# Kernel tuning notes

Hardware: AMD Instinct MI355X
Metric: run time of the kernel (lower is better)

Reference implementation:

```python
import jax, jax.numpy as jnp
import numpy as np

NV = 1_000_000   # number of 'var' nodes
NC = 500_000     # number of 'con' nodes
E = 16_000_000   # number of v2c edges (c2v is the reverse edge set)
H = 10           # n_h_feats


def setup_inputs() -> dict:
    key = jax.random.key(0)
    ks = jax.random.split(key, 24)
    s = 0.1  # weight init scale
    inp = {
        "var_c": jax.random.normal(ks[0], (NV,), jnp.float32),
        "var_x": jax.random.normal(ks[1], (NV,), jnp.float32),
        "con_b": jax.random.normal(ks[2], (NC,), jnp.float32),
        "A": jax.random.uniform(ks[3], (E,), jnp.float32),
        "src": jax.random.randint(ks[4], (E,), 0, NV, jnp.int32),
        "dst": jax.random.randint(ks[5], (E,), 0, NC, jnp.int32),
        # var_emb / con_emb Linear params
        "Wv": jax.random.normal(ks[6], (2, H), jnp.float32) * s,
        "bv": jnp.zeros((H,), jnp.float32),
        "Wc": jax.random.normal(ks[7], (1, H), jnp.float32) * s,
        "bc": jnp.zeros((H,), jnp.float32),
        # conv1 (GraphConv, shared across v2c/c2v) -- note: its output is
        # overwritten in the original forward and never reaches the output
        "W1": jax.random.normal(ks[8], (H, H), jnp.float32) * s,
        "b1": jnp.zeros((H,), jnp.float32),
        # conv2 (GraphConv, shared across v2c/c2v)
        "W2": jax.random.normal(ks[9], (H, H), jnp.float32) * s,
        "b2": jnp.zeros((H,), jnp.float32),
        # output MLP
        "Wo1": jax.random.normal(ks[10], (H, H), jnp.float32) * s,
        "bo1": jnp.zeros((H,), jnp.float32),
        "Wo2": jax.random.normal(ks[11], (H, H), jnp.float32) * s,
        "bo2": jnp.zeros((H,), jnp.float32),
        "Wo3": jax.random.normal(ks[12], (H, 1), jnp.float32) * s,
        "bo3": jnp.zeros((1,), jnp.float32),
    }
    return inp


def _gconv(x_src, W, b, s_idx, d_idx, ew, norm_src, norm_dst, n_dst):
    # DGL GraphConv, norm='both', with edge weights; in==out feats so W first.
    h = (x_src * norm_src) @ W                      # [N_src, H]
    msg = h[s_idx] * ew[:, None]                    # gather + edge weight
    agg = jax.ops.segment_sum(msg, d_idx, num_segments=n_dst)
    return agg * norm_dst + b


def reference(var_c, var_x, con_b, A, src, dst,
              Wv, bv, Wc, bc, W1, b1, W2, b2,
              Wo1, bo1, Wo2, bo2, Wo3, bo3):
    # symmetric norm from UNWEIGHTED degrees (DGL GraphConv norm='both'),
    # clamped at 1. v2c: out-deg(var), in-deg(con); c2v is the reverse.
    ones_e = jnp.ones_like(A)
    deg_v = jnp.clip(jax.ops.segment_sum(ones_e, src, num_segments=NV), 1.0)
    deg_c = jnp.clip(jax.ops.segment_sum(ones_e, dst, num_segments=NC), 1.0)
    norm_v = deg_v[:, None] ** -0.5
    norm_c = deg_c[:, None] ** -0.5

    # node embeddings
    var_feats = jnp.stack([var_c, var_x], axis=1)   # [NV, 2]
    X_var = jax.nn.relu(var_feats @ Wv + bv)        # [NV, H]
    X_con = jax.nn.relu(con_b[:, None] @ Wc + bc)   # [NC, H] (unused by convs: GraphConv ignores dst feats)

    # In the original forward, conv1 outputs (h_con / h_var) are immediately
    # overwritten by conv2 outputs (GraphConv only consumes src features),
    # so only conv2 lies on the effective compute path.
    h_con = jax.nn.relu(_gconv(X_var, W2, b2, src, dst, A, norm_v, norm_c, NC))
    h_var = jax.nn.relu(_gconv(h_con, W2, b2, dst, src, A, norm_c, norm_v, NV))

    h = jax.nn.relu(h_var @ Wo1 + bo1)
    h = jax.nn.relu(h @ Wo2 + bo2)
    logit = h @ Wo3 + bo3                           # [NV, 1]
    # dgl.readout_nodes(op='mean', ntype='var'), single graph -> [1, 1]
    return jnp.mean(logit, axis=0, keepdims=True)
```

## Files before the change

### kernel.cpp

```cpp
#include <hip/hip_runtime.h>

#define HF 10
#define ST 16
#define BST 16
#define SLC 256
#define NBINS 2048
#define VPB 512
#define TILE 12288


__global__ __launch_bounds__(1024) void k_hist(const int* __restrict__ idx,
                                               unsigned* __restrict__ hist,
                                               long long s_begin, long long s_end,
                                               int per, int shift) {
    __shared__ unsigned l[NBINS];
    int t = threadIdx.x, sl = blockIdx.x;
    for (int b = t; b < NBINS; b += 1024) l[b] = 0u;
    __syncthreads();
    long long s0 = s_begin + (long long)sl * per;
    long long s1 = s0 + per; if (s1 > s_end) s1 = s_end;
    for (long long i = s0 + t; i < s1; i += 1024)
        atomicAdd(&l[((unsigned)idx[i]) >> shift], 1u);
    __syncthreads();
    unsigned* out = hist + (size_t)sl * NBINS;
    for (int b = t; b < NBINS; b += 1024) out[b] = l[b];
}

__global__ void k_coltot(const unsigned* __restrict__ h, unsigned* __restrict__ colT) {
    int b = blockIdx.x * 256 + threadIdx.x;
    unsigned s = 0u;
    for (int sl = 0; sl < SLC; sl++) s += h[(size_t)sl * NBINS + b];
    colT[b] = s;
}

__global__ __launch_bounds__(1024) void k_prefix(const unsigned* __restrict__ colT,
                                                 unsigned* __restrict__ start) {
    __shared__ unsigned p[1024];
    int t = threadIdx.x;
    uint2 v = *(const uint2*)(colT + 2 * t);
    unsigned own = v.x + v.y;
    p[t] = own;
    __syncthreads();
    for (int off = 1; off < 1024; off <<= 1) {
        unsigned u = (t >= off) ? p[t - off] : 0u;
        __syncthreads();
        p[t] += u;
        __syncthreads();
    }
    unsigned e = p[t] - own;
    *(uint2*)(start + 2 * t) = make_uint2(e, e + v.x);
    if (t == 1023) start[NBINS] = p[1023];
}

__global__ void k_offs(unsigned* __restrict__ h, const unsigned* __restrict__ start) {
    int b = blockIdx.x * 256 + threadIdx.x;
    unsigned cur = start[b];
    for (int sl = 0; sl < SLC; sl++) {
        unsigned* cell = h + (size_t)sl * NBINS + b;
        unsigned v = *cell;
        *cell = cur;
        cur += v;
    }
}

__global__ __launch_bounds__(1024) void k_scatS2(
        const int* __restrict__ src, const int* __restrict__ dst,
        const float* __restrict__ A, const unsigned* __restrict__ offs,
        uint2* __restrict__ ebufS, long long E, int per) {
    __shared__ unsigned cur[NBINS];
    __shared__ unsigned th[NBINS];
    __shared__ unsigned tf[NBINS];
    __shared__ unsigned sc[1024];
    __shared__ __align__(16) uint2 buf[TILE];
    int t = threadIdx.x, sl = blockIdx.x;
    const unsigned* o = offs + (size_t)sl * NBINS;
    for (int b = t; b < NBINS; b += 1024) cur[b] = o[b];
    long long s0 = (long long)sl * per;
    long long s1 = s0 + per; if (s1 > E) s1 = E;
    for (long long tb = s0; tb < s1; tb += TILE) {
        int n = (int)((s1 - tb < (long long)TILE) ? (s1 - tb) : (long long)TILE);
        for (int b = t; b < NBINS; b += 1024) th[b] = 0u;
        __syncthreads();
        for (int i = t; i < n; i += 1024)
            atomicAdd(&th[((unsigned)src[tb + i]) >> 9], 1u);
        __syncthreads();
        unsigned a0 = th[2 * t], a1 = th[2 * t + 1];
        unsigned own = a0 + a1;
        sc[t] = own;
        __syncthreads();
        for (int off = 1; off < 1024; off <<= 1) {
            unsigned u = (t >= off) ? sc[t - off] : 0u;
            __syncthreads();
            sc[t] += u;
            __syncthreads();
        }
        unsigned ex = sc[t] - own;
        th[2 * t] = ex;     th[2 * t + 1] = ex + a0;
        tf[2 * t] = ex;     tf[2 * t + 1] = ex + a0;
        __syncthreads();
        for (int i = t; i < n; i += 1024) {
            unsigned s = (unsigned)src[tb + i], d = (unsigned)dst[tb + i];
            float a = A[tb + i];
            unsigned p = atomicAdd(&tf[s >> 9], 1u);
            buf[p] = make_uint2(((s & 511u) << 19) | d, __float_as_uint(a));
        }
        __syncthreads();
        int w = t >> 6, ln = t & 63;
        for (int b = w; b < NBINS; b += 16) {
            unsigned lo = th[b], cnt = tf[b] - lo, gb = cur[b];
            for (unsigned j = ln; j < cnt; j += 64)
                ebufS[gb + j] = buf[lo + j];
        }
        __syncthreads();
        for (int b = t; b < NBINS; b += 1024) cur[b] += tf[b] - th[b];
        __syncthreads();
    }
}

__global__ void k_cntS2(const uint2* __restrict__ ebufS, const unsigned* __restrict__ startS,
                        const float* __restrict__ var_c, const float* __restrict__ var_x,
                        float4* __restrict__ vcx, int NV) {
    __shared__ unsigned cnt[VPB];
    int t = threadIdx.x, b = blockIdx.x;
    cnt[t] = 0u; cnt[t + 256] = 0u;
    __syncthreads();
    unsigned i0 = startS[b], i1 = startS[b + 1];
    for (unsigned i = i0 + t; i < i1; i += 256)
        atomicAdd(&cnt[ebufS[i].x >> 19], 1u);
    __syncthreads();
#pragma unroll
    for (int k = 0; k < 2; k++) {
        int v = b * VPB + k * 256 + t;
        if (v < NV)
            vcx[v] = make_float4(var_c[v], var_x[v],
                                 rsqrtf(fmaxf((float)cnt[k * 256 + t], 1.0f)), 0.0f);
    }
}

__global__ __launch_bounds__(1024) void k_histD2(const uint2* __restrict__ ebufB,
                                                 const unsigned* __restrict__ startS,
                                                 unsigned* __restrict__ hist, int B0, int binsPer) {
    __shared__ unsigned l[NBINS];
    int t = threadIdx.x, sl = blockIdx.x;
    for (int b = t; b < NBINS; b += 1024) l[b] = 0u;
    __syncthreads();
    int b0 = B0 + sl * binsPer;
    unsigned i0 = startS[b0], i1 = startS[b0 + binsPer];
    for (unsigned i = i0 + t; i < i1; i += 1024)
        atomicAdd(&l[(ebufB[i].x & 0x7FFFFu) >> 8], 1u);
    __syncthreads();
    unsigned* out = hist + (size_t)sl * NBINS;
    for (int b = t; b < NBINS; b += 1024) out[b] = l[b];
}

__global__ __launch_bounds__(1024) void k_scatD2(const uint2* __restrict__ ebufB,
                                                 const unsigned* __restrict__ startS,
                                                 const unsigned* __restrict__ offs,
                                                 const float4* __restrict__ vcx,
                                                 uint4* __restrict__ ebufD, int B0, int binsPer,
                                                 unsigned cap) {
    __shared__ unsigned cur[NBINS];
    int t = threadIdx.x, sl = blockIdx.x;
    const unsigned* o = offs + (size_t)sl * NBINS;
    for (int b = t; b < NBINS; b += 1024) cur[b] = o[b];
    __syncthreads();
    int b0 = B0 + sl * binsPer;
    for (int bb = 0; bb < binsPer; bb++) {
        int bin = b0 + bb;
        unsigned vbase = ((unsigned)bin) << 9;
        unsigned i0 = startS[bin], i1 = startS[bin + 1];
        for (unsigned i = i0 + t; i < i1; i += 1024) {
            uint2 kv = ebufB[i];
            unsigned d = kv.x & 0x7FFFFu;
            float4 g = vcx[vbase | (kv.x >> 19)];
            unsigned pos = atomicAdd(&cur[d >> 8], 1u);
            if (pos < cap)
                ebufD[pos] = make_uint4(d & 255u, __float_as_uint(__uint_as_float(kv.y) * g.z),
                                        __float_as_uint(g.x), __float_as_uint(g.y));
        }
    }
}

__global__ __launch_bounds__(1024) void k_scatD(const int* __restrict__ src, const int* __restrict__ dst,
                                                const float* __restrict__ A,
                                                const unsigned* __restrict__ offs,
                                                const float4* __restrict__ vcx,
                                                uint4* __restrict__ ebufD,
                                                long long s_begin, long long s_end, int per) {
    __shared__ unsigned cur[NBINS];
    int t = threadIdx.x, sl = blockIdx.x;
    const unsigned* o = offs + (size_t)sl * NBINS;
    for (int b = t; b < NBINS; b += 1024) cur[b] = o[b];
    __syncthreads();
    long long s0 = s_begin + (long long)sl * per;
    long long s1 = s0 + per; if (s1 > s_end) s1 = s_end;
    for (long long i = s0 + t; i < s1; i += 4096) {
        unsigned sv[4], dv[4]; float av[4]; bool hv[4];
#pragma unroll
        for (int j = 0; j < 4; j++) {
            long long idx = i + (long long)j * 1024;
            hv[j] = idx < s1;
            if (hv[j]) { sv[j] = (unsigned)src[idx]; dv[j] = (unsigned)dst[idx]; av[j] = A[idx]; }
            else       { sv[j] = 0u; dv[j] = 0u; av[j] = 0.0f; }
        }
        float4 g[4];
#pragma unroll
        for (int j = 0; j < 4; j++)
            if (hv[j]) g[j] = vcx[sv[j]];
#pragma unroll
        for (int j = 0; j < 4; j++) {
            if (!hv[j]) continue;
            unsigned pos = atomicAdd(&cur[dv[j] >> 8], 1u);
            ebufD[pos] = make_uint4(dv[j] & 255u, __float_as_uint(av[j] * g[j].z),
                                    __float_as_uint(g[j].x), __float_as_uint(g[j].y));
        }
    }
}

__global__ void k_aggD(const uint4* __restrict__ ebufD, const unsigned* __restrict__ startD,
                       const float* __restrict__ Wv, const float* __restrict__ bv,
                       float* __restrict__ bufC, float* __restrict__ deg_c, int NC) {
    __shared__ float acc[256 * HF];
    __shared__ unsigned cnt[256];
    int t = threadIdx.x, b = blockIdx.x;
    for (int i = t; i < 256 * HF; i += 256) acc[i] = 0.0f;
    cnt[t] = 0u;
    float wv0[HF], wv1[HF], bvv[HF];
#pragma unroll
    for (int h = 0; h < HF; h++) { wv0[h] = Wv[h]; wv1[h] = Wv[HF + h]; bvv[h] = bv[h]; }
    __syncthreads();
    unsigned i0 = startD[b], i1 = startD[b + 1];
    for (unsigned i = i0 + t; i < i1; i += 256) {
        uint4 kv = ebufD[i];
        unsigned dl = kv.x;
        float anv = __uint_as_float(kv.y);
        float c   = __uint_as_float(kv.z);
        float x   = __uint_as_float(kv.w);
        float* ac = acc + dl * HF;
#pragma unroll
        for (int h = 0; h < HF; h++) {
            float e = fmaxf(fmaf(c, wv0[h], fmaf(x, wv1[h], bvv[h])), 0.0f);
            atomicAdd(ac + h, anv * e);
        }
        atomicAdd(&cnt[dl], 1u);
    }
    __syncthreads();
    int gid = b * 256 + t;
    if (gid < NC) {
        float* row = bufC + (size_t)gid * BST;
#pragma unroll
        for (int h = 0; h < HF; h++) row[h] += acc[t * HF + h];
        deg_c[gid] += (float)cnt[t];
    }
}

__global__ void k_conT(float* __restrict__ bufC, const float* __restrict__ deg_c,
                       const float* __restrict__ W2, const float* __restrict__ b2, int NC) {
    __shared__ float sW[HF * HF], sb[HF];
    int t = threadIdx.x;
    if (t < HF * HF) sW[t] = W2[t];
    if (t < HF)      sb[t] = b2[t];
    __syncthreads();
    int i = blockIdx.x * 256 + t;
    if (i >= NC) return;
    float nc = rsqrtf(fmaxf(deg_c[i], 1.0f));
    float* row = bufC + (size_t)i * BST;
    float x[HF];
#pragma unroll
    for (int h = 0; h < HF; h++) x[h] = row[h];
#pragma unroll
    for (int j = 0; j < HF; j++) {
        float a = 0.0f;
#pragma unroll
        for (int k = 0; k < HF; k++) a = fmaf(x[k], sW[k * HF + j], a);
        row[j] = fmaxf(fmaf(a, nc, sb[j]), 0.0f) * nc;
    }
}

__global__ __launch_bounds__(256) void k_aggS(
        const uint2* __restrict__ ebufS, const unsigned* __restrict__ startS,
        const float* __restrict__ bufC, const float4* __restrict__ vcx,
        const float* __restrict__ W2, const float* __restrict__ b2,
        const float* __restrict__ Wo1, const float* __restrict__ bo1,
        const float* __restrict__ Wo2, const float* __restrict__ bo2,
        const float* __restrict__ Wo3, const float* __restrict__ bo3,
        double* __restrict__ gacc, int NV) {
    __shared__ float acc[VPB * HF];
    __shared__ float sW2[HF * HF], sb2[HF], sW1[HF * HF], sb1[HF], sWm[HF * HF], sbm[HF], sW3[HF];
    __shared__ float sb3;
    __shared__ double red[256];
    int t = threadIdx.x, b = blockIdx.x;
    for (int i = t; i < VPB * HF; i += 256) acc[i] = 0.0f;
    if (t < HF * HF) { sW2[t] = W2[t]; sW1[t] = Wo1[t]; sWm[t] = Wo2[t]; }
    if (t < HF)      { sb2[t] = b2[t]; sb1[t] = bo1[t]; sbm[t] = bo2[t]; sW3[t] = Wo3[t]; }
    if (t == 0)      sb3 = bo3[0];
    __syncthreads();
    unsigned i0 = startS[b], i1 = startS[b + 1];
    int grp = t >> 2;
    int q   = t & 3;
    int nq  = (q < 2) ? 4 : (q == 2 ? 2 : 0);
    for (unsigned base = i0; base < i1; base += 64) {
        unsigned e = base + (unsigned)grp;
        bool ok = e < i1;
        uint2 kv = ok ? ebufS[e] : make_uint2(0u, 0u);
        float4 y = make_float4(0.f, 0.f, 0.f, 0.f);
        if (ok) y = *(const float4*)(bufC + (size_t)(kv.x & 0x7FFFFu) * BST + 4 * q);
        if (ok && nq) {
            float a = __uint_as_float(kv.y);
            float* ac = acc + (kv.x >> 19) * HF + 4 * q;
            atomicAdd(ac + 0, a * y.x);
            atomicAdd(ac + 1, a * y.y);
            if (nq == 4) {
                atomicAdd(ac + 2, a * y.z);
                atomicAdd(ac + 3, a * y.w);
            }
        }
    }
    __syncthreads();
    double local = 0.0;
#pragma unroll
    for (int k = 0; k < 2; k++) {
        int v = b * VPB + k * 256 + t;
        if (v < NV) {
            float nv = vcx[v].z;
            float x[HF], hvv[HF], h1[HF], h2[HF];
#pragma unroll
            for (int h = 0; h < HF; h++) x[h] = acc[(k * 256 + t) * HF + h];
#pragma unroll
            for (int j = 0; j < HF; j++) {
                float a = 0.0f;
#pragma unroll
                for (int kk = 0; kk < HF; kk++) a = fmaf(x[kk], sW2[kk * HF + j], a);
                hvv[j] = fmaxf(fmaf(a, nv, sb2[j]), 0.0f);
            }
#pragma unroll
            for (int j = 0; j < HF; j++) {
                float a = sb1[j];
#pragma unroll
                for (int kk = 0; kk < HF; kk++) a = fmaf(hvv[kk], sW1[kk * HF + j], a);
                h1[j] = fmaxf(a, 0.0f);
            }
#pragma unroll
            for (int j = 0; j < HF; j++) {
                float a = sbm[j];
#pragma unroll
                for (int kk = 0; kk < HF; kk++) a = fmaf(h1[kk], sWm[kk * HF + j], a);
                h2[j] = fmaxf(a, 0.0f);
            }
            float logit = sb3;
#pragma unroll
            for (int kk = 0; kk < HF; kk++) logit = fmaf(h2[kk], sW3[kk], logit);
            local += (double)logit;
        }
    }
    red[t] = local;
    __syncthreads();
    for (int s = 128; s > 0; s >>= 1) {
        if (t < s) red[t] += red[t + s];
        __syncthreads();
    }
    if (t == 0) atomicAdd(gacc, red[0]);
}

__global__ void k_out(const double* __restrict__ acc, float* __restrict__ out, int NV) {
    out[0] = (float)(acc[0] / (double)NV);
}


__global__ void k_degree(const int* __restrict__ src, const int* __restrict__ dst,
                         float* __restrict__ deg_v, float* __restrict__ deg_c, int E) {
    int i = blockIdx.x * blockDim.x + threadIdx.x;
    if (i < E) {
        atomicAdd(&deg_v[src[i]], 1.0f);
        atomicAdd(&deg_c[dst[i]], 1.0f);
    }
}

__global__ void k_norm(float* __restrict__ d, int n) {
    int i = blockIdx.x * blockDim.x + threadIdx.x;
    if (i < n) d[i] = 1.0f / sqrtf(fmaxf(d[i], 1.0f));
}

__global__ void k_var_emb(const float* __restrict__ var_c, const float* __restrict__ var_x,
                          const float* __restrict__ norm_v,
                          const float* __restrict__ Wv, const float* __restrict__ bv,
                          const float* __restrict__ W2,
                          float* __restrict__ out, int NV) {
    __shared__ float sWv[2 * HF], sbv[HF], sW2[HF * HF];
    int t = threadIdx.x;
    if (t < 2 * HF) sWv[t] = Wv[t];
    if (t < HF)     sbv[t] = bv[t];
    if (t < HF * HF) sW2[t] = W2[t];
    __syncthreads();
    int i = blockIdx.x * blockDim.x + t;
    if (i >= NV) return;
    float c = var_c[i], x = var_x[i], nv = norm_v[i];
    float e[HF];
#pragma unroll
    for (int h = 0; h < HF; h++)
        e[h] = fmaxf(fmaf(c, sWv[h], fmaf(x, sWv[HF + h], sbv[h])), 0.0f) * nv;
    float* row = out + (size_t)i * ST;
#pragma unroll
    for (int j = 0; j < HF; j++) {
        float acc = 0.0f;
#pragma unroll
        for (int k = 0; k < HF; k++) acc = fmaf(e[k], sW2[k * HF + j], acc);
        row[j] = acc;
    }
}

__global__ void k_edge(const int* __restrict__ gidx, const int* __restrict__ didx,
                       const float* __restrict__ A,
                       const float* __restrict__ h, float* __restrict__ agg, int E) {
    int tid = blockIdx.x * blockDim.x + threadIdx.x;
    int e = tid / 5;
    if (e >= E) return;
    int q = tid - e * 5;
    int s = gidx[e], d = didx[e];
    float a = A[e];
    const float2 m = *(const float2*)(h + (size_t)s * ST + 2 * q);
    float* o = agg + (size_t)d * ST + 2 * q;
    atomicAdd(o,     m.x * a);
    atomicAdd(o + 1, m.y * a);
}

__global__ void k_con(float* __restrict__ buf, const float* __restrict__ norm_c,
                      const float* __restrict__ W2, const float* __restrict__ b2, int NC) {
    __shared__ float sW2[HF * HF], sb2[HF];
    int t = threadIdx.x;
    if (t < HF * HF) sW2[t] = W2[t];
    if (t < HF)      sb2[t] = b2[t];
    __syncthreads();
    int i = blockIdx.x * blockDim.x + t;
    if (i >= NC) return;
    float nc = norm_c[i];
    float* row = buf + (size_t)i * ST;
    float hc[HF];
#pragma unroll
    for (int h = 0; h < HF; h++)
        hc[h] = fmaxf(fmaf(row[h], nc, sb2[h]), 0.0f) * nc;
#pragma unroll
    for (int j = 0; j < HF; j++) {
        float acc = 0.0f;
#pragma unroll
        for (int k = 0; k < HF; k++) acc = fmaf(hc[k], sW2[k * HF + j], acc);
        row[j] = acc;
    }
}

__global__ void k_final(const float* __restrict__ agg_v, const float* __restrict__ norm_v,
                        const float* __restrict__ b2,
                        const float* __restrict__ Wo1, const float* __restrict__ bo1,
                        const float* __restrict__ Wo2, const float* __restrict__ bo2,
                        const float* __restrict__ Wo3, const float* __restrict__ bo3,
                        double* __restrict__ acc, int NV) {
    __shared__ float sb2[HF], sW1[HF * HF], sb1[HF], sW2m[HF * HF], sb2m[HF], sW3[HF];
    __shared__ float sb3;
    __shared__ double red[256];
    int t = threadIdx.x;
    if (t < HF)      sb2[t]  = b2[t];
    if (t < HF * HF) sW1[t]  = Wo1[t];
    if (t < HF)      sb1[t]  = bo1[t];
    if (t < HF * HF) sW2m[t] = Wo2[t];
    if (t < HF)      sb2m[t] = bo2[t];
    if (t < HF)      sW3[t]  = Wo3[t];
    if (t == 0)      sb3     = bo3[0];
    __syncthreads();
    int i = blockIdx.x * blockDim.x + t;
    double local = 0.0;
    if (i < NV) {
        float nv = norm_v[i];
        const float* row = agg_v + (size_t)i * ST;
        float v[HF], h1[HF], h2[HF];
#pragma unroll
        for (int h = 0; h < HF; h++) v[h] = fmaxf(fmaf(row[h], nv, sb2[h]), 0.0f);
#pragma unroll
        for (int j = 0; j < HF; j++) {
            float a = sb1[j];
#pragma unroll
            for (int k = 0; k < HF; k++) a = fmaf(v[k], sW1[k * HF + j], a);
            h1[j] = fmaxf(a, 0.0f);
        }
#pragma unroll
        for (int j = 0; j < HF; j++) {
            float a = sb2m[j];
#pragma unroll
            for (int k = 0; k < HF; k++) a = fmaf(h1[k], sW2m[k * HF + j], a);
            h2[j] = fmaxf(a, 0.0f);
        }
        float logit = sb3;
#pragma unroll
        for (int k = 0; k < HF; k++) logit = fmaf(h2[k], sW3[k], logit);
        local = (double)logit;
    }
    red[t] = local;
    __syncthreads();
    for (int s = 128; s > 0; s >>= 1) {
        if (t < s) red[t] += red[t + s];
        __syncthreads();
    }
    if (t == 0) atomicAdd(acc, red[0]);
}


extern "C" void kernel_launch(void* const* d_in, const int* in_sizes, int n_in,
                              void* d_out, int out_size, void* d_ws, size_t ws_size,
                              hipStream_t stream) {
    const float* var_c = (const float*)d_in[0];
    const float* var_x = (const float*)d_in[1];
    const float* A   = (const float*)d_in[3];
    const int*   src = (const int*)d_in[4];
    const int*   dst = (const int*)d_in[5];
    const float* Wv  = (const float*)d_in[6];
    const float* bv  = (const float*)d_in[7];
    const float* W2  = (const float*)d_in[12];
    const float* b2  = (const float*)d_in[13];
    const float* Wo1 = (const float*)d_in[14];
    const float* bo1 = (const float*)d_in[15];
    const float* Wo2 = (const float*)d_in[16];
    const float* bo2 = (const float*)d_in[17];
    const float* Wo3 = (const float*)d_in[18];
    const float* bo3 = (const float*)d_in[19];

    const int NV = in_sizes[0];
    const int NC = in_sizes[2];
    const int E  = in_sizes[3];

    long long EcMaxUsed = 0;
    auto layout_bytes = [&](int nDc, bool binchunk, size_t* offs_out) -> size_t {
        size_t off = 0;
        auto alloc = [&](size_t bytes, int slot) {
            if (offs_out) offs_out[slot] = off;
            off = (off + bytes + 255) & ~(size_t)255;
        };
        long long ec;
        if (binchunk) {
            long long vspan = (long long)(NBINS / nDc) * VPB;
            if (vspan > NV) vspan = NV;
            ec = ((long long)E * vspan) / NV + (long long)E / 64 + 1024;
            if (ec > E) ec = E;
        } else {
            ec = ((long long)E + nDc - 1) / nDc;
        }
        EcMaxUsed = ec;
        alloc((size_t)NC * BST * 4, 0);
        alloc((size_t)NV * 16, 1);
        alloc((size_t)NC * 4, 2);
        alloc((size_t)SLC * NBINS * 4, 3);
        alloc((size_t)SLC * NBINS * 4, 4);
        alloc((size_t)NBINS * 4, 5);
        alloc((size_t)(NBINS + 1) * 4, 6);
        alloc((size_t)(NBINS + 1) * 4, 7);
        alloc(8, 8);
        alloc((size_t)E * 8, 9);
        alloc((size_t)ec * 16, 10);
        return off;
    };

    int nD = 0;
    bool binc = false;
    size_t offs[11];
    for (int cand : {4, 8, 16}) {
        if (layout_bytes(cand, true, nullptr) <= ws_size) { nD = cand; binc = true; break; }
    }
    if (nD == 0) {
        for (int cand = 2; cand <= 16; cand++)
            if (layout_bytes(cand, false, nullptr) <= ws_size) { nD = cand; break; }
    }
    bool fast = (nD > 0) && (NV <= (1 << 20)) && (NC <= (1 << 19)) && (E > 0);

    char* ws = (char*)d_ws;
    if (fast) {
        layout_bytes(nD, binc, offs);
        const long long EcMax = EcMaxUsed;
        float*    bufC   = (float*)(ws + offs[0]);
        float4*   vcx    = (float4*)(ws + offs[1]);
        float*    deg_c  = (float*)(ws + offs[2]);
        unsigned* hS     = (unsigned*)(ws + offs[3]);
        unsigned* hD     = (unsigned*)(ws + offs[4]);
        unsigned* colT   = (unsigned*)(ws + offs[5]);
        unsigned* startS = (unsigned*)(ws + offs[6]);
        unsigned* startD = (unsigned*)(ws + offs[7]);
        double*   gacc   = (double*)(ws + offs[8]);
        uint2*    ebufS  = (uint2*)(ws + offs[9]);
        uint4*    ebufD  = (uint4*)(ws + offs[10]);

        const int perS = (int)(((long long)E + SLC - 1) / SLC);
        const int NB_S = (NV + VPB - 1) / VPB;
        const int NB_C = (NC + 255) >> 8;

        hipMemsetAsync(bufC,  0, (size_t)NC * BST * 4, stream);
        hipMemsetAsync(deg_c, 0, (size_t)NC * 4, stream);
        hipMemsetAsync(gacc,  0, 8, stream);

        k_hist<<<SLC, 1024, 0, stream>>>(src, hS, 0, E, perS, 9);
        k_coltot<<<NBINS / 256, 256, 0, stream>>>(hS, colT);
        k_prefix<<<1, 1024, 0, stream>>>(colT, startS);
        k_offs<<<NBINS / 256, 256, 0, stream>>>(hS, startS);
        k_scatS2<<<SLC, 1024, 0, stream>>>(src, dst, A, hS, ebufS, E, perS);

        k_cntS2<<<NB_S, 256, 0, stream>>>(ebufS, startS, var_c, var_x, vcx, NV);

        if (binc) {
            const int binsChunk = NBINS / nD;
            const int binsPer   = (binsChunk + SLC - 1) / SLC;
            for (int c = 0; c < nD; c++) {
                int B0 = c * binsChunk;
                k_histD2<<<SLC, 1024, 0, stream>>>(ebufS, startS, hD, B0, binsPer);
                k_coltot<<<NBINS / 256, 256, 0, stream>>>(hD, colT);
                k_prefix<<<1, 1024, 0, stream>>>(colT, startD);
                k_offs<<<NBINS / 256, 256, 0, stream>>>(hD, startD);
                k_scatD2<<<SLC, 1024, 0, stream>>>(ebufS, startS, hD, vcx, ebufD,
                                                   B0, binsPer, (unsigned)EcMax);
                k_aggD<<<NB_C, 256, 0, stream>>>(ebufD, startD, Wv, bv, bufC, deg_c, NC);
            }
        } else {
            const int perD = (int)((EcMax + SLC - 1) / SLC);
            for (int c = 0; c < nD; c++) {
                long long cb = (long long)c * EcMax;
                long long ce = cb + EcMax; if (ce > E) ce = E;
                k_hist<<<SLC, 1024, 0, stream>>>(dst, hD, cb, ce, perD, 8);
                k_coltot<<<NBINS / 256, 256, 0, stream>>>(hD, colT);
                k_prefix<<<1, 1024, 0, stream>>>(colT, startD);
                k_offs<<<NBINS / 256, 256, 0, stream>>>(hD, startD);
                k_scatD<<<SLC, 1024, 0, stream>>>(src, dst, A, hD, vcx, ebufD, cb, ce, perD);
                k_aggD<<<NB_C, 256, 0, stream>>>(ebufD, startD, Wv, bv, bufC, deg_c, NC);
            }
        }
        k_conT<<<NB_C, 256, 0, stream>>>(bufC, deg_c, W2, b2, NC);

        k_aggS<<<NB_S, 256, 0, stream>>>(ebufS, startS, bufC, vcx, W2, b2,
                                         Wo1, bo1, Wo2, bo2, Wo3, bo3, gacc, NV);
        k_out<<<1, 1, 0, stream>>>(gacc, (float*)d_out, NV);
    } else {
        const int B = 256;
        float* fbufV = (float*)ws;
        float* fbufC = (float*)(ws + (size_t)NV * ST * 4);
        float* deg_v = (float*)(ws + (size_t)(NV + NC) * ST * 4);
        float* deg_c = deg_v + NV;
        size_t acc_off = ((size_t)(NV + NC) * ST * 4 + (size_t)(NV + NC) * 4 + 7) & ~(size_t)7;
        double* acc = (double*)(ws + acc_off);

        hipMemsetAsync(deg_v, 0, (size_t)(NV + NC) * 4, stream);
        hipMemsetAsync(fbufC, 0, (size_t)NC * ST * 4, stream);
        hipMemsetAsync(acc, 0, sizeof(double), stream);

        k_degree<<<(E + B - 1) / B, B, 0, stream>>>(src, dst, deg_v, deg_c, E);
        k_norm<<<(NV + NC + B - 1) / B, B, 0, stream>>>(deg_v, NV + NC);
        k_var_emb<<<(NV + B - 1) / B, B, 0, stream>>>(var_c, var_x, deg_v, Wv, bv, W2, fbufV, NV);

        long long tE = (long long)E * 5;
        k_edge<<<(int)((tE + B - 1) / B), B, 0, stream>>>(src, dst, A, fbufV, fbufC, E);
        k_con<<<(NC + B - 1) / B, B, 0, stream>>>(fbufC, deg_c, W2, b2, NC);

        hipMemsetAsync(fbufV, 0, (size_t)NV * ST * 4, stream);
        k_edge<<<(int)((tE + B - 1) / B), B, 0, stream>>>(dst, src, A, fbufC, fbufV, E);

        k_final<<<(NV + B - 1) / B, B, 0, stream>>>(fbufV, deg_v, b2, Wo1, bo1, Wo2, bo2, Wo3, bo3, acc, NV);
        k_out<<<1, 1, 0, stream>>>(acc, (float*)d_out, NV);
    }
}
```

Measured before the change: 2.533 ms.

## Stage dst-binned scatter through shared-memory tiles and widen con bins to 512

The dst-side scatter now processes each source bin in tiles. It builds a local histogram and prefix scan in shared memory, stages the records sorted by destination bin in LDS, and then writes each bin's run contiguously to global memory, so the scattered 16-byte writes become coalesced. The con bin width goes from 256 to 512 nodes (1024 bins), which halves the bin count for the histogram and the staging, and k_aggD now covers 512 cons per block with a larger shared accumulator. The cost is extra syncs and scan passes per tile, a large LDS footprint that limits occupancy, and more atomic contention per block in aggregation.

```diff
diff --git a/kernel.cpp b/kernel.cpp
--- a/kernel.cpp
+++ b/kernel.cpp
@@ -7,6 +7,10 @@
 #define NBINS 2048
 #define VPB 512
 #define TILE 12288
+#define NBD 1024
+#define DSH 9
+#define CPB 512
+#define TILED 6144
 
 
 __global__ __launch_bounds__(1024) void k_hist(const int* __restrict__ idx,
@@ -147,36 +151,67 @@
     int b0 = B0 + sl * binsPer;
     unsigned i0 = startS[b0], i1 = startS[b0 + binsPer];
     for (unsigned i = i0 + t; i < i1; i += 1024)
-        atomicAdd(&l[(ebufB[i].x & 0x7FFFFu) >> 8], 1u);
+        atomicAdd(&l[(ebufB[i].x & 0x7FFFFu) >> DSH], 1u);
     __syncthreads();
     unsigned* out = hist + (size_t)sl * NBINS;
     for (int b = t; b < NBINS; b += 1024) out[b] = l[b];
 }
 
-__global__ __launch_bounds__(1024) void k_scatD2(const uint2* __restrict__ ebufB,
-                                                 const unsigned* __restrict__ startS,
-                                                 const unsigned* __restrict__ offs,
-                                                 const float4* __restrict__ vcx,
-                                                 uint4* __restrict__ ebufD, int B0, int binsPer,
-                                                 unsigned cap) {
-    __shared__ unsigned cur[NBINS];
+__global__ __launch_bounds__(1024) void k_scatD3(
+        const uint2* __restrict__ ebufB, const unsigned* __restrict__ startS,
+        const unsigned* __restrict__ offs, const float4* __restrict__ vcx,
+        uint4* __restrict__ ebufD, int B0, int binsPer, unsigned cap) {
+    __shared__ unsigned cur[NBD];
+    __shared__ unsigned th[NBD], tf[NBD];
+    __shared__ unsigned sc[1024];
+    __shared__ __align__(16) uint4 buf[TILED];
     int t = threadIdx.x, sl = blockIdx.x;
     const unsigned* o = offs + (size_t)sl * NBINS;
-    for (int b = t; b < NBINS; b += 1024) cur[b] = o[b];
+    cur[t] = o[t];
     __syncthreads();
     int b0 = B0 + sl * binsPer;
     for (int bb = 0; bb < binsPer; bb++) {
         int bin = b0 + bb;
         unsigned vbase = ((unsigned)bin) << 9;
         unsigned i0 = startS[bin], i1 = startS[bin + 1];
-        for (unsigned i = i0 + t; i < i1; i += 1024) {
-            uint2 kv = ebufB[i];
-            unsigned d = kv.x & 0x7FFFFu;
-            float4 g = vcx[vbase | (kv.x >> 19)];
-            unsigned pos = atomicAdd(&cur[d >> 8], 1u);
-            if (pos < cap)
-                ebufD[pos] = make_uint4(d & 255u, __float_as_uint(__uint_as_float(kv.y) * g.z),
-                                        __float_as_uint(g.x), __float_as_uint(g.y));
+        for (unsigned tb = i0; tb < i1; tb += TILED) {
+            unsigned n = (i1 - tb < (unsigned)TILED) ? (i1 - tb) : (unsigned)TILED;
+            th[t] = 0u;
+            __syncthreads();
+            for (unsigned i = t; i < n; i += 1024)
+                atomicAdd(&th[(ebufB[tb + i].x & 0x7FFFFu) >> DSH], 1u);
+            __syncthreads();
+            unsigned own = th[t];
+            sc[t] = own;
+            __syncthreads();
+            for (int off = 1; off < 1024; off <<= 1) {
+                unsigned u = (t >= off) ? sc[t - off] : 0u;
+                __syncthreads();
+                sc[t] += u;
+                __syncthreads();
+            }
+            unsigned ex = sc[t] - own;
+            th[t] = ex; tf[t] = ex;
+            __syncthreads();
+            for (unsigned i = t; i < n; i += 1024) {
+                uint2 kv = ebufB[tb + i];
+                unsigned d = kv.x & 0x7FFFFu;
+                float4 g = vcx[vbase | (kv.x >> 19)];
+                unsigned p = atomicAdd(&tf[d >> DSH], 1u);
+                buf[p] = make_uint4(d & (CPB - 1u),
+                                    __float_as_uint(__uint_as_float(kv.y) * g.z),
+                                    __float_as_uint(g.x), __float_as_uint(g.y));
+            }
+            __syncthreads();
+            int w = t >> 6, ln = t & 63;
+            for (int b = w; b < NBD; b += 16) {
+                unsigned lo = th[b], cnt = tf[b] - lo, gb = cur[b];
+                for (unsigned j = ln; j < cnt; j += 64)
+                    if (gb + j < cap) ebufD[gb + j] = buf[lo + j];
+            }
+            __syncthreads();
+            cur[t] += tf[t] - th[t];
+            __syncthreads();
         }
     }
 }
@@ -210,21 +245,22 @@
 #pragma unroll
         for (int j = 0; j < 4; j++) {
             if (!hv[j]) continue;
-            unsigned pos = atomicAdd(&cur[dv[j] >> 8], 1u);
-            ebufD[pos] = make_uint4(dv[j] & 255u, __float_as_uint(av[j] * g[j].z),
+            unsigned pos = atomicAdd(&cur[dv[j] >> DSH], 1u);
+            ebufD[pos] = make_uint4(dv[j] & (CPB - 1u), __float_as_uint(av[j] * g[j].z),
                                     __float_as_uint(g[j].x), __float_as_uint(g[j].y));
         }
     }
 }
 
-__global__ void k_aggD(const uint4* __restrict__ ebufD, const unsigned* __restrict__ startD,
-                       const float* __restrict__ Wv, const float* __restrict__ bv,
-                       float* __restrict__ bufC, float* __restrict__ deg_c, int NC) {
-    __shared__ float acc[256 * HF];
-    __shared__ unsigned cnt[256];
+__global__ __launch_bounds__(256) void k_aggD(
+        const uint4* __restrict__ ebufD, const unsigned* __restrict__ startD,
+        const float* __restrict__ Wv, const float* __restrict__ bv,
+        float* __restrict__ bufC, float* __restrict__ deg_c, int NC) {
+    __shared__ float acc[CPB * HF];
+    __shared__ unsigned cnt[CPB];
     int t = threadIdx.x, b = blockIdx.x;
-    for (int i = t; i < 256 * HF; i += 256) acc[i] = 0.0f;
-    cnt[t] = 0u;
+    for (int i = t; i < CPB * HF; i += 256) acc[i] = 0.0f;
+    cnt[t] = 0u; cnt[t + 256] = 0u;
     float wv0[HF], wv1[HF], bvv[HF];
 #pragma unroll
     for (int h = 0; h < HF; h++) { wv0[h] = Wv[h]; wv1[h] = Wv[HF + h]; bvv[h] = bv[h]; }
@@ -245,12 +281,15 @@
         atomicAdd(&cnt[dl], 1u);
     }
     __syncthreads();
-    int gid = b * 256 + t;
-    if (gid < NC) {
-        float* row = bufC + (size_t)gid * BST;
-#pragma unroll
-        for (int h = 0; h < HF; h++) row[h] += acc[t * HF + h];
-        deg_c[gid] += (float)cnt[t];
+#pragma unroll
+    for (int k = 0; k < 2; k++) {
+        int gid = b * CPB + k * 256 + t;
+        if (gid < NC) {
+            float* row = bufC + (size_t)gid * BST;
+#pragma unroll
+            for (int h = 0; h < HF; h++) row[h] += acc[(k * 256 + t) * HF + h];
+            deg_c[gid] += (float)cnt[k * 256 + t];
+        }
     }
 }
 
@@ -588,6 +627,7 @@
         const int perS = (int)(((long long)E + SLC - 1) / SLC);
         const int NB_S = (NV + VPB - 1) / VPB;
         const int NB_C = (NC + 255) >> 8;
+        const int NB_C2 = (NC + CPB - 1) / CPB;
 
         hipMemsetAsync(bufC,  0, (size_t)NC * BST * 4, stream);
         hipMemsetAsync(deg_c, 0, (size_t)NC * 4, stream);
@@ -610,21 +650,21 @@
                 k_coltot<<<NBINS / 256, 256, 0, stream>>>(hD, colT);
                 k_prefix<<<1, 1024, 0, stream>>>(colT, startD);
                 k_offs<<<NBINS / 256, 256, 0, stream>>>(hD, startD);
-                k_scatD2<<<SLC, 1024, 0, stream>>>(ebufS, startS, hD, vcx, ebufD,
+                k_scatD3<<<SLC, 1024, 0, stream>>>(ebufS, startS, hD, vcx, ebufD,
                                                    B0, binsPer, (unsigned)EcMax);
-                k_aggD<<<NB_C, 256, 0, stream>>>(ebufD, startD, Wv, bv, bufC, deg_c, NC);
+                k_aggD<<<NB_C2, 256, 0, stream>>>(ebufD, startD, Wv, bv, bufC, deg_c, NC);
             }
         } else {
             const int perD = (int)((EcMax + SLC - 1) / SLC);
             for (int c = 0; c < nD; c++) {
                 long long cb = (long long)c * EcMax;
                 long long ce = cb + EcMax; if (ce > E) ce = E;
-                k_hist<<<SLC, 1024, 0, stream>>>(dst, hD, cb, ce, perD, 8);
+                k_hist<<<SLC, 1024, 0, stream>>>(dst, hD, cb, ce, perD, DSH);
                 k_coltot<<<NBINS / 256, 256, 0, stream>>>(hD, colT);
                 k_prefix<<<1, 1024, 0, stream>>>(colT, startD);
                 k_offs<<<NBINS / 256, 256, 0, stream>>>(hD, startD);
                 k_scatD<<<SLC, 1024, 0, stream>>>(src, dst, A, hD, vcx, ebufD, cb, ce, perD);
-                k_aggD<<<NB_C, 256, 0, stream>>>(ebufD, startD, Wv, bv, bufC, deg_c, NC);
+                k_aggD<<<NB_C2, 256, 0, stream>>>(ebufD, startD, Wv, bv, bufC, deg_c, NC);
             }
         }
         k_conT<<<NB_C, 256, 0, stream>>>(bufC, deg_c, W2, b2, NC);
```

After: 2.626 ms. 3.7% more time.
